# Kernel optimization log

Hardware: AMD Instinct MI355X
Metric: run time of the kernel (lower is better)

Reference implementation:

```python
import jax, jax.numpy as jnp
import numpy as np


def relu_bt(x):
    # -threshold(-leaky_relu(x), -t, -t) == min(leaky_relu(x), t), t = ||x||_inf (detached)
    t = jax.lax.stop_gradient(jnp.max(jnp.abs(x)))
    return jnp.minimum(jax.nn.leaky_relu(x, negative_slope=0.01), t)


def setup_inputs() -> dict:
    key = jax.random.key(0)
    k1, k2, k3, k4 = jax.random.split(key, 4)
    N, E, F_in, F_out = 100000, 1600000, 128, 64
    x = jax.random.normal(k1, (N, F_in), dtype=jnp.float32)
    edge_index = jax.random.randint(k2, (2, E), 0, N, dtype=jnp.int64)
    # xavier_normal with gain=1.414
    W = jax.random.normal(k3, (F_in, F_out), dtype=jnp.float32) * (1.414 * np.sqrt(2.0 / (F_in + F_out)))
    a = jax.random.normal(k4, (1, 4 * F_out), dtype=jnp.float32) * (1.414 * np.sqrt(2.0 / (1 + 4 * F_out)))
    return {"x": x, "edge_index": edge_index, "W": W, "a": a}


def reference(x, edge_index, W, a):
    N = x.shape[0]
    F_out = W.shape[1]
    h = x @ W  # [N, F_out]
    src = edge_index[0]
    dst = edge_index[1]
    hs = h[src]  # [E, F_out]
    hd = h[dst]  # [E, F_out]
    agg = relu_bt(hs + hd)
    diff = relu_bt(hs - hd)
    # a @ cat([hs, hd, agg, diff], dim=1).T == sum of four per-edge dot products
    a0, a1, a2, a3 = jnp.split(a.reshape(4 * F_out), 4)
    score = hs @ a0 + hd @ a1 + agg @ a2 + diff @ a3  # [E]
    edge_e = jnp.exp(-relu_bt(score))  # [E]
    # spmm(A, ones): rowsum over outgoing edges (grouped by src)
    e_rowsum = jax.ops.segment_sum(edge_e, src, num_segments=N)  # [N]
    # spmm(A, h): weighted aggregation of neighbor (dst) features into src rows
    h_prime = jax.ops.segment_sum(edge_e[:, None] * hd, src, num_segments=N)  # [N, F_out]
    return h_prime / (e_rowsum[:, None] + 1e-16)
```

## Files before the change

kernel.cpp:

```cpp
#include <hip/hip_runtime.h>
#include <hip/hip_fp16.h>

#define F_IN 128
#define F_OUT 64
#define BIN_TILE 2048
#define BSHIFT 8
#define BNODES 256
#define BCAP 6144u

#define LK_A 0.505f
#define LK_B 0.495f

__device__ __forceinline__ float leaky(float v) {
    return fmaf(LK_B, fabsf(v), LK_A * v);
}

template <int CTRL>
__device__ __forceinline__ float dppadd(float v) {
    return v + __builtin_bit_cast(float,
        __builtin_amdgcn_update_dpp(0, __builtin_bit_cast(int, v), CTRL, 0xf, 0xf, true));
}

__device__ __forceinline__ float sum8(float v) {
    v = dppadd<0xB1>(v);
    v = dppadd<0x4E>(v);
    v = dppadd<0x141>(v);
    return v;
}

__device__ __forceinline__ float xslot_sum2(float v) {
    v = dppadd<0x128>(v);
    v += __shfl_xor(v, 16);
    return v;
}

__device__ __forceinline__ float wave_sum(float v) {
    v += __builtin_bit_cast(float, __builtin_amdgcn_update_dpp(0, __builtin_bit_cast(int, v), 0x111, 0xf, 0xf, true));
    v += __builtin_bit_cast(float, __builtin_amdgcn_update_dpp(0, __builtin_bit_cast(int, v), 0x112, 0xf, 0xf, true));
    v += __builtin_bit_cast(float, __builtin_amdgcn_update_dpp(0, __builtin_bit_cast(int, v), 0x114, 0xf, 0xe, true));
    v += __builtin_bit_cast(float, __builtin_amdgcn_update_dpp(0, __builtin_bit_cast(int, v), 0x118, 0xf, 0xc, true));
    v += __builtin_bit_cast(float, __builtin_amdgcn_update_dpp(0, __builtin_bit_cast(int, v), 0x142, 0xa, 0xf, true));
    v += __builtin_bit_cast(float, __builtin_amdgcn_update_dpp(0, __builtin_bit_cast(int, v), 0x143, 0xc, 0xf, true));
    return __builtin_bit_cast(float, __builtin_amdgcn_readlane(__builtin_bit_cast(int, v), 63));
}

__device__ __forceinline__ void cvt8(const uint4 u, float* g) {
    float2 f;
    f = __half22float2(__builtin_bit_cast(__half2, u.x)); g[0] = f.x; g[1] = f.y;
    f = __half22float2(__builtin_bit_cast(__half2, u.y)); g[2] = f.x; g[3] = f.y;
    f = __half22float2(__builtin_bit_cast(__half2, u.z)); g[4] = f.x; g[5] = f.y;
    f = __half22float2(__builtin_bit_cast(__half2, u.w)); g[6] = f.x; g[7] = f.y;
}

__global__ __launch_bounds__(256) void gemm_xw(const float* __restrict__ x,
                                               const float* __restrict__ W,
                                               float* __restrict__ h32,
                                               uint2* __restrict__ h16,
                                               unsigned* __restrict__ gcur,
                                               int N, int NB, unsigned cap, int mode) {
    if (gcur && blockIdx.x == 0)
        for (int i = threadIdx.x; i < NB; i += 256) gcur[i] = (unsigned)i * cap;

    __shared__ float w_lds[F_IN][F_OUT];
    {
        const float4* Wv = (const float4*)W;
        float4* wl = (float4*)w_lds;
        for (int i = threadIdx.x; i < F_IN * F_OUT / 4; i += 256) wl[i] = Wv[i];
    }
    __syncthreads();

    const int cg = threadIdx.x & 15;
    const int rs = threadIdx.x >> 4;
    const int row0 = blockIdx.x * 64 + rs * 4;

    int r[4];
#pragma unroll
    for (int i = 0; i < 4; ++i) { const int rr = row0 + i; r[i] = rr < N ? rr : N - 1; }

    float4 acc[4];
#pragma unroll
    for (int i = 0; i < 4; ++i) acc[i] = make_float4(0.f, 0.f, 0.f, 0.f);

    float4 xc[4];
#pragma unroll
    for (int i = 0; i < 4; ++i) xc[i] = *(const float4*)(x + (size_t)r[i] * F_IN);

    for (int k4 = 0; k4 < 32; ++k4) {
        float4 xn[4];
        if (k4 < 31) {
#pragma unroll
            for (int i = 0; i < 4; ++i)
                xn[i] = *(const float4*)(x + (size_t)r[i] * F_IN + (k4 + 1) * 4);
        }
        float4 wv[4];
#pragma unroll
        for (int kk = 0; kk < 4; ++kk)
            wv[kk] = *(const float4*)&w_lds[k4 * 4 + kk][cg * 4];

#pragma unroll
        for (int i = 0; i < 4; ++i) {
            acc[i].x = fmaf(xc[i].x, wv[0].x, acc[i].x);
            acc[i].y = fmaf(xc[i].x, wv[0].y, acc[i].y);
            acc[i].z = fmaf(xc[i].x, wv[0].z, acc[i].z);
            acc[i].w = fmaf(xc[i].x, wv[0].w, acc[i].w);
            acc[i].x = fmaf(xc[i].y, wv[1].x, acc[i].x);
            acc[i].y = fmaf(xc[i].y, wv[1].y, acc[i].y);
            acc[i].z = fmaf(xc[i].y, wv[1].z, acc[i].z);
            acc[i].w = fmaf(xc[i].y, wv[1].w, acc[i].w);
            acc[i].x = fmaf(xc[i].z, wv[2].x, acc[i].x);
            acc[i].y = fmaf(xc[i].z, wv[2].y, acc[i].y);
            acc[i].z = fmaf(xc[i].z, wv[2].z, acc[i].z);
            acc[i].w = fmaf(xc[i].z, wv[2].w, acc[i].w);
            acc[i].x = fmaf(xc[i].w, wv[3].x, acc[i].x);
            acc[i].y = fmaf(xc[i].w, wv[3].y, acc[i].y);
            acc[i].z = fmaf(xc[i].w, wv[3].z, acc[i].z);
            acc[i].w = fmaf(xc[i].w, wv[3].w, acc[i].w);
        }
        if (k4 < 31) {
#pragma unroll
            for (int i = 0; i < 4; ++i) xc[i] = xn[i];
        }
    }

#pragma unroll
    for (int i = 0; i < 4; ++i) {
        const int rr = row0 + i;
        if (rr < N) {
            if (mode & 2) *(float4*)(h32 + (size_t)rr * F_OUT + cg * 4) = acc[i];
            if (mode & 1) {
                uint2 u;
                u.x = __builtin_bit_cast(unsigned, __floats2half2_rn(acc[i].x, acc[i].y));
                u.y = __builtin_bit_cast(unsigned, __floats2half2_rn(acc[i].z, acc[i].w));
                h16[(size_t)rr * 16 + cg] = u;
            }
        }
    }
}

__global__ __launch_bounds__(256) void binA(const int* __restrict__ ei,
                                            unsigned* __restrict__ gcur,
                                            unsigned* __restrict__ binned,
                                            int E, int NB, unsigned cap) {
    __shared__ unsigned lcnt[1024];
    __shared__ unsigned lbase[1024];
    const int t = threadIdx.x;
    for (int i = t; i < NB; i += 256) lcnt[i] = 0;
    __syncthreads();
    const int base = blockIdx.x * BIN_TILE;
    unsigned pk[8], bk[8], rk[8];
#pragma unroll
    for (int i = 0; i < 8; ++i) {
        const int e = base + i * 256 + t;
        if (e < E) {
            const unsigned s = (unsigned)ei[e];
            const unsigned d = (unsigned)ei[E + e];
            bk[i] = s >> BSHIFT;
            pk[i] = ((s & (BNODES - 1u)) << 17) | d;
            rk[i] = atomicAdd(&lcnt[bk[i]], 1u);
        }
    }
    __syncthreads();
    for (int i = t; i < NB; i += 256) {
        const unsigned c = lcnt[i];
        lbase[i] = c ? atomicAdd(&gcur[i], c) : 0u;
    }
    __syncthreads();
#pragma unroll
    for (int i = 0; i < 8; ++i) {
        const int e = base + i * 256 + t;
        if (e < E) {
            const unsigned pos = lbase[bk[i]] + rk[i];
            if (pos < (bk[i] + 1u) * cap) binned[pos] = pk[i];
        }
    }
}

__global__ __launch_bounds__(256) void scan_counts(const unsigned* __restrict__ gcur,
                                                   unsigned* __restrict__ bcnt,
                                                   unsigned* __restrict__ bbase,
                                                   int NB, unsigned cap) {
    __shared__ unsigned v[1024];
    __shared__ unsigned ts[256];
    const int t = threadIdx.x;
    for (int i = t; i < 1024; i += 256) {
        unsigned c = 0;
        if (i < NB) { c = gcur[i] - (unsigned)i * cap; if (c > cap) c = cap; }
        v[i] = c;
    }
    __syncthreads();
    unsigned s = 0;
#pragma unroll
    for (int j = 0; j < 4; ++j) s += v[t * 4 + j];
    ts[t] = s;
    __syncthreads();
    for (int st = 1; st < 256; st <<= 1) {
        const unsigned add = (t >= st) ? ts[t - st] : 0u;
        __syncthreads();
        ts[t] += add;
        __syncthreads();
    }
    unsigned run = (t > 0) ? ts[t - 1] : 0u;
#pragma unroll
    for (int j = 0; j < 4; ++j) {
        const int i = t * 4 + j;
        const unsigned c = v[i];
        if (i < NB) { bcnt[i] = c; bbase[i] = run; }
        run += c;
    }
}

__global__ __launch_bounds__(256) void binB(const unsigned* __restrict__ binned,
                                            const unsigned* __restrict__ bbase,
                                            const unsigned* __restrict__ bcnt,
                                            unsigned* __restrict__ off,
                                            int* __restrict__ sdst,
                                            int N, int NB, unsigned cap) {
    __shared__ unsigned stg[BCAP];
    __shared__ unsigned ncnt[BNODES];
    __shared__ unsigned ts[256];
    const int b = blockIdx.x;
    const int t = threadIdx.x;
    const unsigned src0 = (unsigned)b * cap;
    const unsigned beg = bbase[b];
    unsigned sz = bcnt[b]; if (sz > BCAP) sz = BCAP;

    ncnt[t] = 0;
    for (unsigned i = t; i < sz; i += 256) stg[i] = binned[src0 + i];
    __syncthreads();

    for (unsigned i = t; i < sz; i += 256) atomicAdd(&ncnt[stg[i] >> 17], 1u);
    __syncthreads();

    const unsigned myc = ncnt[t];
    ts[t] = myc;
    __syncthreads();
    for (int st = 1; st < 256; st <<= 1) {
        const unsigned add = (t >= st) ? ts[t - st] : 0u;
        __syncthreads();
        ts[t] += add;
        __syncthreads();
    }
    const unsigned excl = ts[t] - myc;
    ncnt[t] = excl;
    const int g = (b << BSHIFT) + t;
    if (g < N) off[g] = beg + excl;
    if (b == NB - 1 && t == 0) off[N] = beg + ts[255];
    __syncthreads();

    for (unsigned i = t; i < sz; i += 256) {
        const unsigned p = stg[i];
        const unsigned pos = atomicAdd(&ncnt[p >> 17], 1u);
        sdst[beg + pos] = (int)(p & 0x1FFFFu);
    }
}

__global__ __launch_bounds__(256) void node_kernel(const unsigned* __restrict__ off,
                                                   const int* __restrict__ sdst,
                                                   const uint2* __restrict__ h16v,
                                                   const float* __restrict__ a,
                                                   float* __restrict__ out, int N) {
    const int lane  = threadIdx.x & 63;
    const int half  = lane >> 5;
    const int slot4 = (lane >> 3) & 3;
    const int q     = lane & 7;
    const char* h16 = (const char*)h16v;

    float b1[8], a2b[8], a3b[8], a0m[8];
#pragma unroll
    for (int f = 0; f < 8; ++f) {
        const float A0 = a[q * 8 + f];
        const float A1 = a[64 + q * 8 + f];
        const float A2 = a[128 + q * 8 + f];
        const float A3 = a[192 + q * 8 + f];
        b1[f]  = fmaf(LK_A, A2 - A3, A1);
        a2b[f] = LK_B * A2;
        a3b[f] = LK_B * A3;
        a0m[f] = fmaf(LK_A, A2 + A3, A0);
    }

    const int wid = (int)((blockIdx.x * 256u + threadIdx.x) >> 6);
    const int nw  = (int)((gridDim.x * 256u) >> 6);

    for (int pr = wid; pr * 2 < N; pr += nw) {
        const int node = pr * 2 + half;
        const int nc = (node < N) ? node : N - 1;
        const int beg = (int)off[nc];
        const int len = (node < N) ? ((int)off[nc + 1] - beg) : 0;

        float hs[8];
        {
            const uint4 u = *(const uint4*)(h16 + ((size_t)nc << 7) + q * 16);
            cvt8(u, hs);
        }
        float csp = 0.f;
#pragma unroll
        for (int f = 0; f < 8; ++f) csp = fmaf(hs[f], a0m[f], csp);
        const float cs = sum8(csp);

        const int lenO = __shfl_xor(len, 32);
        const int ml = (len > lenO) ? len : lenO;

        float acc[8];
#pragma unroll
        for (int f = 0; f < 8; ++f) acc[f] = 0.f;
        float rsum = 0.f;

        const int lm1 = (len > 0) ? len - 1 : 0;
        int dA = 0;
        if (len > 0) { int e0 = slot4;      if (e0 > lm1) e0 = lm1; dA = sdst[beg + e0]; }
        uint4 uA = *(const uint4*)(h16 + ((size_t)dA << 7) + q * 16);
        int dB = dA;
        if (len > 4)  { int e1 = 4 + slot4;  if (e1 > lm1) e1 = lm1; dB = sdst[beg + e1]; }
        uint4 uB = *(const uint4*)(h16 + ((size_t)dB << 7) + q * 16);
        int dC = dB;
        if (len > 8)  { int e2 = 8 + slot4;  if (e2 > lm1) e2 = lm1; dC = sdst[beg + e2]; }

        for (int cb = 0; cb < ml; cb += 4) {
            uint4 uC = uB;
            int dD = dC;
            if (cb + 8 < len)
                uC = *(const uint4*)(h16 + ((size_t)dC << 7) + q * 16);
            if (cb + 12 < len) { int e3 = cb + 12 + slot4; if (e3 > lm1) e3 = lm1; dD = sdst[beg + e3]; }

            float g[8];
            cvt8(uA, g);
            float p0 = 0.f, p1 = 0.f;
#pragma unroll
            for (int f = 0; f < 8; f += 2) {
                const float sa0 = hs[f] + g[f],         sb0 = hs[f] - g[f];
                const float sa1 = hs[f + 1] + g[f + 1], sb1 = hs[f + 1] - g[f + 1];
                p0 = fmaf(g[f],     b1[f],     p0);
                p1 = fmaf(g[f + 1], b1[f + 1], p1);
                p0 = fmaf(fabsf(sa0), a2b[f],     p0);
                p1 = fmaf(fabsf(sa1), a2b[f + 1], p1);
                p0 = fmaf(fabsf(sb0), a3b[f],     p0);
                p1 = fmaf(fabsf(sb1), a3b[f + 1], p1);
            }
            const float R = sum8(p0 + p1);

            float e = __expf(-leaky(cs + R));
            e = (cb + slot4 < len) ? e : 0.f;
#pragma unroll
            for (int f = 0; f < 8; ++f) acc[f] = fmaf(e, g[f], acc[f]);
            rsum += e;

            uA = uB; uB = uC; dC = dD;
        }

#pragma unroll
        for (int f = 0; f < 8; ++f) acc[f] = xslot_sum2(acc[f]);
        rsum = xslot_sum2(rsum);

        if (slot4 == 0 && node < N) {
            const float inv = 1.f / (rsum + 1e-16f);
            float4 o0, o1;
            o0.x = acc[0] * inv; o0.y = acc[1] * inv; o0.z = acc[2] * inv; o0.w = acc[3] * inv;
            o1.x = acc[4] * inv; o1.y = acc[5] * inv; o1.z = acc[6] * inv; o1.w = acc[7] * inv;
            float* orow = out + (size_t)node * F_OUT + q * 8;
            *(float4*)orow = o0;
            *(float4*)(orow + 4) = o1;
        }
    }
}

__global__ __launch_bounds__(256) void hist_kernel(const int* __restrict__ ei,
                                                   unsigned* __restrict__ cnt, int E) {
    const int e = blockIdx.x * 256 + threadIdx.x;
    if (e < E) atomicAdd(&cnt[ei[e]], 1u);
}

__global__ __launch_bounds__(256) void scan1(const unsigned* __restrict__ cnt,
                                             unsigned* __restrict__ bsum, int n) {
    __shared__ unsigned lds[256];
    const int t = threadIdx.x;
    const int base = blockIdx.x * 2048 + t * 8;
    unsigned s = 0;
#pragma unroll
    for (int i = 0; i < 8; ++i) { const int idx = base + i; if (idx < n) s += cnt[idx]; }
    lds[t] = s; __syncthreads();
    for (int st = 128; st > 0; st >>= 1) {
        if (t < st) lds[t] += lds[t + st];
        __syncthreads();
    }
    if (t == 0) bsum[blockIdx.x] = lds[0];
}

__global__ __launch_bounds__(128) void scan2(unsigned* __restrict__ bsum,
                                             unsigned* __restrict__ off, int nb, int n) {
    __shared__ unsigned lds[128];
    const int t = threadIdx.x;
    if (t < nb) lds[t] = bsum[t];
    __syncthreads();
    if (t == 0) {
        unsigned run = 0;
        for (int i = 0; i < nb; ++i) { const unsigned v = lds[i]; lds[i] = run; run += v; }
        off[n] = run;
    }
    __syncthreads();
    if (t < nb) bsum[t] = lds[t];
}

__global__ __launch_bounds__(256) void scan3(const unsigned* __restrict__ cnt,
                                             const unsigned* __restrict__ bsum,
                                             unsigned* __restrict__ off,
                                             unsigned* __restrict__ cursor, int n) {
    __shared__ unsigned lds[256];
    const int t = threadIdx.x;
    const int base = blockIdx.x * 2048 + t * 8;
    unsigned v[8]; unsigned s = 0;
#pragma unroll
    for (int i = 0; i < 8; ++i) { const int idx = base + i; v[i] = (idx < n) ? cnt[idx] : 0u; s += v[i]; }
    lds[t] = s; __syncthreads();
    for (int st = 1; st < 256; st <<= 1) {
        const unsigned add = (t >= st) ? lds[t - st] : 0u;
        __syncthreads();
        lds[t] += add;
        __syncthreads();
    }
    unsigned excl = (t > 0 ? lds[t - 1] : 0u) + bsum[blockIdx.x];
#pragma unroll
    for (int i = 0; i < 8; ++i) {
        const int idx = base + i;
        if (idx < n) { off[idx] = excl; cursor[idx] = excl; excl += v[i]; }
    }
}

__global__ __launch_bounds__(256) void scatter_kernel(const int* __restrict__ ei,
                                                      unsigned* __restrict__ cursor,
                                                      int* __restrict__ sdst, int E) {
    const int e = blockIdx.x * 256 + threadIdx.x;
    if (e >= E) return;
    const int s = ei[e];
    const int d = ei[E + e];
    const unsigned pos = atomicAdd(&cursor[s], 1u);
    sdst[pos] = d;
}

__device__ __forceinline__ float edge_part(float hs, float hd, float a1, float a2, float a3) {
    float p = hd * a1;
    p = fmaf(leaky(hs + hd), a2, p);
    p = fmaf(leaky(hs - hd), a3, p);
    return p;
}

__global__ __launch_bounds__(256) void edge_kernel(const int* __restrict__ ei,
                                                   const float* __restrict__ h,
                                                   const float* __restrict__ a,
                                                   float* __restrict__ hprime,
                                                   float* __restrict__ rowsum,
                                                   int E) {
    const int lane = threadIdx.x & 63;
    const int wave = (int)((blockIdx.x * blockDim.x + threadIdx.x) >> 6);
    const int nwaves = (int)((gridDim.x * blockDim.x) >> 6);
    const float a0 = a[lane], a1 = a[64 + lane], a2 = a[128 + lane], a3 = a[192 + lane];
    for (int e = wave; e < E; e += nwaves) {
        const int s = ei[e];
        const int d = ei[E + e];
        const float hs = h[(size_t)s * F_OUT + lane];
        const float hd = h[(size_t)d * F_OUT + lane];
        const float part = wave_sum(hs * a0 + edge_part(hs, hd, a1, a2, a3));
        const float ee = __expf(-leaky(part));
        atomicAdd(&hprime[(size_t)s * F_OUT + lane], ee * hd);
        if (lane == 0) atomicAdd(&rowsum[s], ee);
    }
}

__global__ __launch_bounds__(256) void finalize(float* __restrict__ out,
                                                const float* __restrict__ rowsum,
                                                int total) {
    const int i = blockIdx.x * blockDim.x + threadIdx.x;
    if (i < total) out[i] = out[i] / (rowsum[i >> 6] + 1e-16f);
}

static inline size_t align_up(size_t v, size_t a) { return (v + a - 1) & ~(a - 1); }

extern "C" void kernel_launch(void* const* d_in, const int* in_sizes, int n_in,
                              void* d_out, int out_size, void* d_ws, size_t ws_size,
                              hipStream_t stream) {
    const float* x  = (const float*)d_in[0];
    const int*   ei = (const int*)d_in[1];
    const float* W  = (const float*)d_in[2];
    const float* a  = (const float*)d_in[3];

    const int N = in_sizes[0] / F_IN;
    const int E = in_sizes[1] / 2;
    float* out = (float*)d_out;

    const int NB = (N + BNODES - 1) >> BSHIFT;
    const int ngemm = (N + 63) / 64;
    const int nbt = (E + BIN_TILE - 1) / BIN_TILE;
    const unsigned meanFill = (NB > 0) ? (unsigned)(E / NB) : 0u;

    char* ws = (char*)d_ws;
    const size_t szh16  = align_up((size_t)N * F_OUT * 2, 256);
    const size_t szoff  = align_up(((size_t)N + 1) * 4, 256);
    const size_t szedge = align_up((size_t)E * 4 + 64, 256);
    const size_t szbin  = align_up((size_t)NB * BCAP * 4 + 64, 256);

    const size_t off_b  = szh16;
    const size_t sdst_b = off_b + szoff;
    const size_t binned_b = sdst_b + szedge;
    const size_t gcur_b   = binned_b + szbin;
    const size_t bcnt_b   = gcur_b + 4096;
    const size_t bbase_b  = bcnt_b + 4096;
    const size_t needA    = bbase_b + 4096;
    const size_t cursor_b = sdst_b + szedge;
    const size_t cnt_b    = cursor_b + align_up((size_t)N * 4, 256);
    const size_t bsum_b   = cnt_b + align_up((size_t)N * 4, 256);
    const size_t needB    = bsum_b + 4096;

    uint2* h16 = (uint2*)ws;
    const int nodeBlocks = 2048;

    if (ws_size >= needA && N <= (1 << 17) && NB <= 1024 && meanFill <= (BCAP * 3u) / 4u) {
        unsigned* off    = (unsigned*)(ws + off_b);
        int*      sdst   = (int*)(ws + sdst_b);
        unsigned* binned = (unsigned*)(ws + binned_b);
        unsigned* gcur   = (unsigned*)(ws + gcur_b);
        unsigned* bcnt   = (unsigned*)(ws + bcnt_b);
        unsigned* bbase  = (unsigned*)(ws + bbase_b);

        gemm_xw<<<ngemm, 256, 0, stream>>>(x, W, nullptr, h16, gcur, N, NB, BCAP, 1);
        binA<<<nbt, 256, 0, stream>>>(ei, gcur, binned, E, NB, BCAP);
        scan_counts<<<1, 256, 0, stream>>>(gcur, bcnt, bbase, NB, BCAP);
        binB<<<NB, 256, 0, stream>>>(binned, bbase, bcnt, off, sdst, N, NB, BCAP);
        node_kernel<<<nodeBlocks, 256, 0, stream>>>(off, sdst, h16, a, out, N);
    } else if (ws_size >= needB && N <= (1 << 17)) {
        unsigned* off    = (unsigned*)(ws + off_b);
        int*      sdst   = (int*)(ws + sdst_b);
        unsigned* cursor = (unsigned*)(ws + cursor_b);
        unsigned* cnt    = (unsigned*)(ws + cnt_b);
        unsigned* bsum   = (unsigned*)(ws + bsum_b);
        const int nb2 = (N + 2047) / 2048;

        hipMemsetAsync(cnt, 0, (size_t)N * 4, stream);
        gemm_xw<<<ngemm, 256, 0, stream>>>(x, W, nullptr, h16, nullptr, N, NB, BCAP, 1);
        hist_kernel<<<(E + 255) / 256, 256, 0, stream>>>(ei, cnt, E);
        scan1<<<nb2, 256, 0, stream>>>(cnt, bsum, N);
        scan2<<<1, 128, 0, stream>>>(bsum, off, nb2, N);
        scan3<<<nb2, 256, 0, stream>>>(cnt, bsum, off, cursor, N);
        scatter_kernel<<<(E + 255) / 256, 256, 0, stream>>>(ei, cursor, sdst, E);
        node_kernel<<<nodeBlocks, 256, 0, stream>>>(off, sdst, h16, a, out, N);
    } else {
        float* h32    = (float*)ws;
        float* rowsum = (float*)(ws + align_up((size_t)N * F_OUT * 4, 256));
        hipMemsetAsync(d_out, 0, (size_t)N * F_OUT * sizeof(float), stream);
        hipMemsetAsync(rowsum, 0, (size_t)N * sizeof(float), stream);
        gemm_xw<<<ngemm, 256, 0, stream>>>(x, W, h32, nullptr, nullptr, N, NB, BCAP, 2);
        edge_kernel<<<2048, 256, 0, stream>>>(ei, h32, a, out, rowsum, E);
        finalize<<<((size_t)N * F_OUT + 255) / 256, 256, 0, stream>>>(out, rowsum, N * F_OUT);
    }
}
```

Measured before the change: 144.6 us.

## Drop scan kernel via padded per-bin CSR, prefetch next node, widen GEMM tile

```diff
diff --git a/kernel.cpp b/kernel.cpp
--- a/kernel.cpp
+++ b/kernel.cpp
@@ -71,25 +71,25 @@
 
     const int cg = threadIdx.x & 15;
     const int rs = threadIdx.x >> 4;
-    const int row0 = blockIdx.x * 64 + rs * 4;
-
-    int r[4];
-#pragma unroll
-    for (int i = 0; i < 4; ++i) { const int rr = row0 + i; r[i] = rr < N ? rr : N - 1; }
-
-    float4 acc[4];
-#pragma unroll
-    for (int i = 0; i < 4; ++i) acc[i] = make_float4(0.f, 0.f, 0.f, 0.f);
-
-    float4 xc[4];
-#pragma unroll
-    for (int i = 0; i < 4; ++i) xc[i] = *(const float4*)(x + (size_t)r[i] * F_IN);
+    const int row0 = blockIdx.x * 128 + rs * 8;
+
+    int r[8];
+#pragma unroll
+    for (int i = 0; i < 8; ++i) { const int rr = row0 + i; r[i] = rr < N ? rr : N - 1; }
+
+    float4 acc[8];
+#pragma unroll
+    for (int i = 0; i < 8; ++i) acc[i] = make_float4(0.f, 0.f, 0.f, 0.f);
+
+    float4 xc[8];
+#pragma unroll
+    for (int i = 0; i < 8; ++i) xc[i] = *(const float4*)(x + (size_t)r[i] * F_IN);
 
     for (int k4 = 0; k4 < 32; ++k4) {
-        float4 xn[4];
+        float4 xn[8];
         if (k4 < 31) {
 #pragma unroll
-            for (int i = 0; i < 4; ++i)
+            for (int i = 0; i < 8; ++i)
                 xn[i] = *(const float4*)(x + (size_t)r[i] * F_IN + (k4 + 1) * 4);
         }
         float4 wv[4];
@@ -98,7 +98,7 @@
             wv[kk] = *(const float4*)&w_lds[k4 * 4 + kk][cg * 4];
 
 #pragma unroll
-        for (int i = 0; i < 4; ++i) {
+        for (int i = 0; i < 8; ++i) {
             acc[i].x = fmaf(xc[i].x, wv[0].x, acc[i].x);
             acc[i].y = fmaf(xc[i].x, wv[0].y, acc[i].y);
             acc[i].z = fmaf(xc[i].x, wv[0].z, acc[i].z);
@@ -118,12 +118,12 @@
         }
         if (k4 < 31) {
 #pragma unroll
-            for (int i = 0; i < 4; ++i) xc[i] = xn[i];
-        }
-    }
-
-#pragma unroll
-    for (int i = 0; i < 4; ++i) {
+            for (int i = 0; i < 8; ++i) xc[i] = xn[i];
+        }
+    }
+
+#pragma unroll
+    for (int i = 0; i < 8; ++i) {
         const int rr = row0 + i;
         if (rr < N) {
             if (mode & 2) *(float4*)(h32 + (size_t)rr * F_OUT + cg * 4) = acc[i];
@@ -175,44 +175,10 @@
     }
 }
 
-__global__ __launch_bounds__(256) void scan_counts(const unsigned* __restrict__ gcur,
-                                                   unsigned* __restrict__ bcnt,
-                                                   unsigned* __restrict__ bbase,
-                                                   int NB, unsigned cap) {
-    __shared__ unsigned v[1024];
-    __shared__ unsigned ts[256];
-    const int t = threadIdx.x;
-    for (int i = t; i < 1024; i += 256) {
-        unsigned c = 0;
-        if (i < NB) { c = gcur[i] - (unsigned)i * cap; if (c > cap) c = cap; }
-        v[i] = c;
-    }
-    __syncthreads();
-    unsigned s = 0;
-#pragma unroll
-    for (int j = 0; j < 4; ++j) s += v[t * 4 + j];
-    ts[t] = s;
-    __syncthreads();
-    for (int st = 1; st < 256; st <<= 1) {
-        const unsigned add = (t >= st) ? ts[t - st] : 0u;
-        __syncthreads();
-        ts[t] += add;
-        __syncthreads();
-    }
-    unsigned run = (t > 0) ? ts[t - 1] : 0u;
-#pragma unroll
-    for (int j = 0; j < 4; ++j) {
-        const int i = t * 4 + j;
-        const unsigned c = v[i];
-        if (i < NB) { bcnt[i] = c; bbase[i] = run; }
-        run += c;
-    }
-}
-
 __global__ __launch_bounds__(256) void binB(const unsigned* __restrict__ binned,
-                                            const unsigned* __restrict__ bbase,
-                                            const unsigned* __restrict__ bcnt,
+                                            const unsigned* __restrict__ gcur,
                                             unsigned* __restrict__ off,
+                                            unsigned* __restrict__ deg,
                                             int* __restrict__ sdst,
                                             int N, int NB, unsigned cap) {
     __shared__ unsigned stg[BCAP];
@@ -221,8 +187,7 @@
     const int b = blockIdx.x;
     const int t = threadIdx.x;
     const unsigned src0 = (unsigned)b * cap;
-    const unsigned beg = bbase[b];
-    unsigned sz = bcnt[b]; if (sz > BCAP) sz = BCAP;
+    unsigned sz = gcur[b] - src0; if (sz > cap) sz = cap;
 
     ncnt[t] = 0;
     for (unsigned i = t; i < sz; i += 256) stg[i] = binned[src0 + i];
@@ -243,18 +208,18 @@
     const unsigned excl = ts[t] - myc;
     ncnt[t] = excl;
     const int g = (b << BSHIFT) + t;
-    if (g < N) off[g] = beg + excl;
-    if (b == NB - 1 && t == 0) off[N] = beg + ts[255];
+    if (g < N) { off[g] = src0 + excl; deg[g] = myc; }
     __syncthreads();
 
     for (unsigned i = t; i < sz; i += 256) {
         const unsigned p = stg[i];
         const unsigned pos = atomicAdd(&ncnt[p >> 17], 1u);
-        sdst[beg + pos] = (int)(p & 0x1FFFFu);
+        sdst[src0 + pos] = (int)(p & 0x1FFFFu);
     }
 }
 
 __global__ __launch_bounds__(256) void node_kernel(const unsigned* __restrict__ off,
+                                                   const unsigned* __restrict__ deg,
                                                    const int* __restrict__ sdst,
                                                    const uint2* __restrict__ h16v,
                                                    const float* __restrict__ a,
@@ -281,17 +246,38 @@
     const int wid = (int)((blockIdx.x * 256u + threadIdx.x) >> 6);
     const int nw  = (int)((gridDim.x * 256u) >> 6);
 
-    for (int pr = wid; pr * 2 < N; pr += nw) {
-        const int node = pr * 2 + half;
-        const int nc = (node < N) ? node : N - 1;
-        const int beg = (int)off[nc];
-        const int len = (node < N) ? ((int)off[nc + 1] - beg) : 0;
-
-        float hs[8];
-        {
-            const uint4 u = *(const uint4*)(h16 + ((size_t)nc << 7) + q * 16);
-            cvt8(u, hs);
-        }
+    int pr = wid;
+    if (pr * 2 >= N) return;
+
+    int node = pr * 2 + half;
+    int nc = (node < N) ? node : N - 1;
+    unsigned bg  = off[nc];
+    unsigned dgv = (node < N) ? deg[nc] : 0u;
+    uint4 hsu = *(const uint4*)(h16 + ((size_t)nc << 7) + q * 16);
+    int dA0 = 0;
+    {
+        const int len0 = (int)dgv;
+        if (len0 > 0) { int e0 = slot4; const int lm = len0 - 1; if (e0 > lm) e0 = lm; dA0 = sdst[bg + e0]; }
+    }
+
+    while (true) {
+        const int prn = pr + nw;
+        const bool hasNext = (prn * 2 < N);
+
+        const int len = (int)dgv;
+        const unsigned beg = bg;
+        float hs[8]; cvt8(hsu, hs);
+
+        int noden = 0, ncn = 0; unsigned bgn = 0, dgn = 0;
+        uint4 hsun = make_uint4(0u, 0u, 0u, 0u);
+        if (hasNext) {
+            noden = prn * 2 + half;
+            ncn = (noden < N) ? noden : N - 1;
+            bgn = off[ncn];
+            dgn = (noden < N) ? deg[ncn] : 0u;
+            hsun = *(const uint4*)(h16 + ((size_t)ncn << 7) + q * 16);
+        }
+
         float csp = 0.f;
 #pragma unroll
         for (int f = 0; f < 8; ++f) csp = fmaf(hs[f], a0m[f], csp);
@@ -306,14 +292,12 @@
         float rsum = 0.f;
 
         const int lm1 = (len > 0) ? len - 1 : 0;
-        int dA = 0;
-        if (len > 0) { int e0 = slot4;      if (e0 > lm1) e0 = lm1; dA = sdst[beg + e0]; }
-        uint4 uA = *(const uint4*)(h16 + ((size_t)dA << 7) + q * 16);
-        int dB = dA;
-        if (len > 4)  { int e1 = 4 + slot4;  if (e1 > lm1) e1 = lm1; dB = sdst[beg + e1]; }
+        uint4 uA = *(const uint4*)(h16 + ((size_t)dA0 << 7) + q * 16);
+        int dB = dA0;
+        if (len > 4) { int e1 = 4 + slot4; if (e1 > lm1) e1 = lm1; dB = sdst[beg + e1]; }
         uint4 uB = *(const uint4*)(h16 + ((size_t)dB << 7) + q * 16);
         int dC = dB;
-        if (len > 8)  { int e2 = 8 + slot4;  if (e2 > lm1) e2 = lm1; dC = sdst[beg + e2]; }
+        if (len > 8) { int e2 = 8 + slot4; if (e2 > lm1) e2 = lm1; dC = sdst[beg + e2]; }
 
         for (int cb = 0; cb < ml; cb += 4) {
             uint4 uC = uB;
@@ -347,6 +331,12 @@
             uA = uB; uB = uC; dC = dD;
         }
 
+        int dA0n = 0;
+        if (hasNext) {
+            const int lenn = (int)dgn;
+            if (lenn > 0) { int e0 = slot4; const int lm = lenn - 1; if (e0 > lm) e0 = lm; dA0n = sdst[bgn + e0]; }
+        }
+
 #pragma unroll
         for (int f = 0; f < 8; ++f) acc[f] = xslot_sum2(acc[f]);
         rsum = xslot_sum2(rsum);
@@ -360,6 +350,9 @@
             *(float4*)orow = o0;
             *(float4*)(orow + 4) = o1;
         }
+
+        if (!hasNext) break;
+        pr = prn; node = noden; nc = ncn; bg = bgn; dgv = dgn; hsu = hsun; dA0 = dA0n;
     }
 }
 
@@ -487,7 +480,7 @@
     float* out = (float*)d_out;
 
     const int NB = (N + BNODES - 1) >> BSHIFT;
-    const int ngemm = (N + 63) / 64;
+    const int ngemm = (N + 127) / 128;
     const int nbt = (E + BIN_TILE - 1) / BIN_TILE;
     const unsigned meanFill = (NB > 0) ? (unsigned)(E / NB) : 0u;
 
@@ -498,13 +491,13 @@
     const size_t szbin  = align_up((size_t)NB * BCAP * 4 + 64, 256);
 
     const size_t off_b  = szh16;
-    const size_t sdst_b = off_b + szoff;
-    const size_t binned_b = sdst_b + szedge;
+    const size_t deg_b    = off_b + szoff;
+    const size_t sdstA_b  = deg_b + szoff;
+    const size_t binned_b = sdstA_b + szbin;
     const size_t gcur_b   = binned_b + szbin;
-    const size_t bcnt_b   = gcur_b + 4096;
-    const size_t bbase_b  = bcnt_b + 4096;
-    const size_t needA    = bbase_b + 4096;
-    const size_t cursor_b = sdst_b + szedge;
+    const size_t needA    = gcur_b + 4096;
+    const size_t sdstB_b  = off_b + szoff;
+    const size_t cursor_b = sdstB_b + szedge;
     const size_t cnt_b    = cursor_b + align_up((size_t)N * 4, 256);
     const size_t bsum_b   = cnt_b + align_up((size_t)N * 4, 256);
     const size_t needB    = bsum_b + 4096;
@@ -514,20 +507,18 @@
 
     if (ws_size >= needA && N <= (1 << 17) && NB <= 1024 && meanFill <= (BCAP * 3u) / 4u) {
         unsigned* off    = (unsigned*)(ws + off_b);
-        int*      sdst   = (int*)(ws + sdst_b);
+        unsigned* deg    = (unsigned*)(ws + deg_b);
+        int*      sdst   = (int*)(ws + sdstA_b);
         unsigned* binned = (unsigned*)(ws + binned_b);
         unsigned* gcur   = (unsigned*)(ws + gcur_b);
-        unsigned* bcnt   = (unsigned*)(ws + bcnt_b);
-        unsigned* bbase  = (unsigned*)(ws + bbase_b);
 
         gemm_xw<<<ngemm, 256, 0, stream>>>(x, W, nullptr, h16, gcur, N, NB, BCAP, 1);
         binA<<<nbt, 256, 0, stream>>>(ei, gcur, binned, E, NB, BCAP);
-        scan_counts<<<1, 256, 0, stream>>>(gcur, bcnt, bbase, NB, BCAP);
-        binB<<<NB, 256, 0, stream>>>(binned, bbase, bcnt, off, sdst, N, NB, BCAP);
-        node_kernel<<<nodeBlocks, 256, 0, stream>>>(off, sdst, h16, a, out, N);
+        binB<<<NB, 256, 0, stream>>>(binned, gcur, off, deg, sdst, N, NB, BCAP);
+        node_kernel<<<nodeBlocks, 256, 0, stream>>>(off, deg, sdst, h16, a, out, N);
     } else if (ws_size >= needB && N <= (1 << 17)) {
         unsigned* off    = (unsigned*)(ws + off_b);
-        int*      sdst   = (int*)(ws + sdst_b);
+        int*      sdst   = (int*)(ws + sdstB_b);
         unsigned* cursor = (unsigned*)(ws + cursor_b);
         unsigned* cnt    = (unsigned*)(ws + cnt_b);
         unsigned* bsum   = (unsigned*)(ws + bsum_b);
@@ -540,7 +531,7 @@
         scan2<<<1, 128, 0, stream>>>(bsum, off, nb2, N);
         scan3<<<nb2, 256, 0, stream>>>(cnt, bsum, off, cursor, N);
         scatter_kernel<<<(E + 255) / 256, 256, 0, stream>>>(ei, cursor, sdst, E);
-        node_kernel<<<nodeBlocks, 256, 0, stream>>>(off, sdst, h16, a, out, N);
+        node_kernel<<<nodeBlocks, 256, 0, stream>>>(off, cnt, sdst, h16, a, out, N);
     } else {
         float* h32    = (float*)ws;
         float* rowsum = (float*)(ws + align_up((size_t)N * F_OUT * 4, 256));
```

Measured after the change: 147.5 us. 2.0% more time.
